# Kernel tuning notes

Hardware: AMD Instinct MI355X
Metric: run time of the kernel (lower is better)

The kernel has to match this reference:

```python
import jax, jax.numpy as jnp
import numpy as np

EPS = 1e-08


def _similarity_transform(S1, S2):
    """Batched Procrustes: S1, S2 are [B, 3, N]. Returns aligned S1_hat [B, 3, N]."""
    mu1 = jnp.mean(S1, axis=-1, keepdims=True)          # [B,3,1]
    mu2 = jnp.mean(S2, axis=-1, keepdims=True)
    X1 = S1 - mu1
    X2 = S2 - mu2
    var1 = jnp.sum(X1 * X1, axis=(1, 2))                # [B]
    # cross-covariance K = X1 @ X2^T + eps (eps added to every entry, as in torch ref)
    K = jnp.einsum('bin,bjn->bij', X1, X2) + EPS        # [B,3,3]
    U, s, Vh = jnp.linalg.svd(K, full_matrices=False)
    V = jnp.swapaxes(Vh, -1, -2)
    # det(U @ V^T) = det(U @ Vh); sign has zero gradient, same as torch
    sign = jax.lax.stop_gradient(jnp.sign(jnp.linalg.det(jnp.matmul(U, Vh))))  # [B]
    ones = jnp.ones_like(sign)
    d = jnp.stack([ones, ones, sign], axis=-1)          # diag of Z, [B,3]
    # R = V @ Z @ U^T
    R = jnp.einsum('bik,bk,bjk->bij', V, d, U)          # [B,3,3]
    scale = jnp.einsum('bij,bji->b', R, K) / var1       # trace(R@K)/var1, [B]
    t = mu2 - scale[:, None, None] * jnp.matmul(R, mu1)  # [B,3,1]
    S1_hat = scale[:, None, None] * jnp.matmul(R, S1) + t
    return S1_hat


def setup_inputs() -> dict:
    key = jax.random.key(0)
    k1, k2 = jax.random.split(key)
    B, N = 1024, 6890
    pred = jax.random.normal(k1, (B, N, 3), dtype=jnp.float32)
    gt = jax.random.normal(k2, (B, N, 3), dtype=jnp.float32)
    return {"pred": pred, "gt": gt}


def reference(pred, gt):
    # inputs are [B, N, 3] -> torch code transposes to [B, 3, N] and back
    S1 = jnp.swapaxes(pred, 1, 2)
    S2 = jnp.swapaxes(gt, 1, 2)
    S1_hat = jnp.swapaxes(_similarity_transform(S1, S2), 1, 2)  # [B,N,3]
    # loss_type == 'l1', reduction='none'
    return jnp.abs(S1_hat - gt)
```

## Files before the change

kernel.cpp:

```cpp
#include <hip/hip_runtime.h>
#include <math.h>

#define NPTS 6890
#define BATCH 1024
#define FLOATS_PER_BATCH (NPTS * 3)
#define NGROUPS 1722

__device__ __forceinline__ void accum(float* acc, float p0, float p1, float p2,
                                      float g0, float g1, float g2) {
  acc[0] += p0;  acc[1] += p1;  acc[2] += p2;
  acc[3] += g0;  acc[4] += g1;  acc[5] += g2;
  acc[6] += p0 * p0 + p1 * p1 + p2 * p2;
  acc[7]  += p0 * g0;  acc[8]  += p0 * g1;  acc[9]  += p0 * g2;
  acc[10] += p1 * g0;  acc[11] += p1 * g1;  acc[12] += p1 * g2;
  acc[13] += p2 * g0;  acc[14] += p2 * g1;  acc[15] += p2 * g2;
}

__global__ __launch_bounds__(256) void reduce_kernel(
    const float* __restrict__ pred, const float* __restrict__ gt,
    float* __restrict__ sums) {
  const int b = blockIdx.x;
  const size_t ofs0 = (size_t)b * FLOATS_PER_BATCH;
  const int skip = (b & 1) ? 2 : 0;
  const size_t ofs = ofs0 + (size_t)skip * 3;
  const float4* __restrict__ p4 = (const float4*)(pred + ofs);
  const float4* __restrict__ g4 = (const float4*)(gt + ofs);

  float acc[16];
#pragma unroll
  for (int i = 0; i < 16; ++i) acc[i] = 0.f;

  for (int gi = threadIdx.x; gi < NGROUPS; gi += 256) {
    const float4 a0 = p4[3 * gi], a1 = p4[3 * gi + 1], a2 = p4[3 * gi + 2];
    const float4 c0 = g4[3 * gi], c1 = g4[3 * gi + 1], c2 = g4[3 * gi + 2];
    accum(acc, a0.x, a0.y, a0.z, c0.x, c0.y, c0.z);
    accum(acc, a0.w, a1.x, a1.y, c0.w, c1.x, c1.y);
    accum(acc, a1.z, a1.w, a2.x, c1.z, c1.w, c2.x);
    accum(acc, a2.y, a2.z, a2.w, c2.y, c2.z, c2.w);
  }

  if (threadIdx.x < 2) {
    const int n = skip ? (int)threadIdx.x : (NPTS - 2 + (int)threadIdx.x);
    const float* pp = pred + ofs0 + 3 * n;
    const float* gg = gt + ofs0 + 3 * n;
    accum(acc, pp[0], pp[1], pp[2], gg[0], gg[1], gg[2]);
  }

#pragma unroll
  for (int i = 0; i < 16; ++i) {
#pragma unroll
    for (int off = 32; off > 0; off >>= 1)
      acc[i] += __shfl_down(acc[i], off, 64);
  }

  __shared__ float red[4][16];
  const int wave = threadIdx.x >> 6;
  const int lane = threadIdx.x & 63;
  if (lane == 0) {
#pragma unroll
    for (int i = 0; i < 16; ++i) red[wave][i] = acc[i];
  }
  __syncthreads();
  if (threadIdx.x < 16) {
    const int i = threadIdx.x;
    sums[b * 16 + i] = red[0][i] + red[1][i] + red[2][i] + red[3][i];
  }
}

__global__ void solve_kernel(const float* __restrict__ sums,
                             float* __restrict__ params) {
  const int b = blockIdx.x * blockDim.x + threadIdx.x;
  if (b >= BATCH) return;
  const float* s = sums + b * 16;
  const double Ninv = 1.0 / (double)NPTS;

  double sp[3] = {s[0], s[1], s[2]};
  double sg[3] = {s[3], s[4], s[5]};
  double mu1[3], mu2[3];
#pragma unroll
  for (int i = 0; i < 3; ++i) { mu1[i] = sp[i] * Ninv; mu2[i] = sg[i] * Ninv; }
  const double var1 =
      (double)s[6] - (sp[0] * sp[0] + sp[1] * sp[1] + sp[2] * sp[2]) * Ninv;

  double K[3][3];
#pragma unroll
  for (int i = 0; i < 3; ++i)
#pragma unroll
    for (int j = 0; j < 3; ++j)
      K[i][j] = (double)s[7 + 3 * i + j] - sp[i] * sg[j] * Ninv + 1e-8;

  double A[3][3];
#pragma unroll
  for (int i = 0; i < 3; ++i)
#pragma unroll
    for (int j = 0; j < 3; ++j)
      A[i][j] = K[0][i] * K[0][j] + K[1][i] * K[1][j] + K[2][i] * K[2][j];

  double V[3][3] = {{1, 0, 0}, {0, 1, 0}, {0, 0, 1}};
  for (int sweep = 0; sweep < 30; ++sweep) {
    const double off = A[0][1] * A[0][1] + A[0][2] * A[0][2] + A[1][2] * A[1][2];
    const double nrm = A[0][0] + A[1][1] + A[2][2];
    if (off <= 1e-30 * nrm * nrm) break;
    for (int pq = 0; pq < 3; ++pq) {
      const int p = (pq == 2) ? 1 : 0;
      const int q = (pq == 0) ? 1 : 2;
      const double apq = A[p][q];
      if (apq == 0.0) continue;
      const double theta = (A[q][q] - A[p][p]) / (2.0 * apq);
      const double tt =
          ((theta >= 0.0) ? 1.0 : -1.0) / (fabs(theta) + sqrt(theta * theta + 1.0));
      const double c = 1.0 / sqrt(tt * tt + 1.0);
      const double sn = tt * c;
      const double app = A[p][p], aqq = A[q][q];
      A[p][p] = app - tt * apq;
      A[q][q] = aqq + tt * apq;
      A[p][q] = 0.0; A[q][p] = 0.0;
      const int r = 3 - p - q;
      const double arp = A[r][p], arq = A[r][q];
      A[r][p] = c * arp - sn * arq; A[p][r] = A[r][p];
      A[r][q] = sn * arp + c * arq; A[q][r] = A[r][q];
#pragma unroll
      for (int k = 0; k < 3; ++k) {
        const double vkp = V[k][p], vkq = V[k][q];
        V[k][p] = c * vkp - sn * vkq;
        V[k][q] = sn * vkp + c * vkq;
      }
    }
  }

  double w[3] = {A[0][0], A[1][1], A[2][2]};
  int i0 = 0, i1 = 1, i2 = 2, tmp;
  if (w[i0] < w[i1]) { tmp = i0; i0 = i1; i1 = tmp; }
  if (w[i0] < w[i2]) { tmp = i0; i0 = i2; i2 = tmp; }
  if (w[i1] < w[i2]) { tmp = i1; i1 = i2; i2 = tmp; }
  const double sv0 = sqrt(fmax(w[i0], 0.0));
  const double sv1 = sqrt(fmax(w[i1], 0.0));
  const double sv2 = sqrt(fmax(w[i2], 0.0));

  const double detK =
      K[0][0] * (K[1][1] * K[2][2] - K[1][2] * K[2][1]) -
      K[0][1] * (K[1][0] * K[2][2] - K[1][2] * K[2][0]) +
      K[0][2] * (K[1][0] * K[2][1] - K[1][1] * K[2][0]);
  const double sgn = (detK > 0.0) ? 1.0 : ((detK < 0.0) ? -1.0 : 0.0);

  const double floor0 = sv0 * 1e-12 + 1e-300;
  const double z0 = 1.0 / fmax(sv0, floor0);
  const double z1 = 1.0 / fmax(sv1, floor0);
  const double z2 = sgn / fmax(sv2, floor0);

  double W[3][3];
#pragma unroll
  for (int a = 0; a < 3; ++a)
#pragma unroll
    for (int c = 0; c < 3; ++c)
      W[a][c] = V[a][i0] * V[c][i0] * z0 + V[a][i1] * V[c][i1] * z1 +
                V[a][i2] * V[c][i2] * z2;

  double R[3][3];
#pragma unroll
  for (int a = 0; a < 3; ++a)
#pragma unroll
    for (int c = 0; c < 3; ++c)
      R[a][c] = W[a][0] * K[c][0] + W[a][1] * K[c][1] + W[a][2] * K[c][2];

  const double trace = sv0 + sv1 + sgn * sv2;
  const double scale = trace / var1;

  float* pr = params + b * 12;
#pragma unroll
  for (int a = 0; a < 3; ++a) {
#pragma unroll
    for (int c = 0; c < 3; ++c) pr[3 * a + c] = (float)(scale * R[a][c]);
    pr[9 + a] = (float)(mu2[a] - scale * (R[a][0] * mu1[0] + R[a][1] * mu1[1] +
                                          R[a][2] * mu1[2]));
  }
}

__device__ __forceinline__ void xform(const float* m, float p0, float p1,
                                      float p2, float g0, float g1, float g2,
                                      float& o0, float& o1, float& o2) {
  o0 = fabsf(m[0] * p0 + m[1] * p1 + m[2] * p2 + m[9] - g0);
  o1 = fabsf(m[3] * p0 + m[4] * p1 + m[5] * p2 + m[10] - g1);
  o2 = fabsf(m[6] * p0 + m[7] * p1 + m[8] * p2 + m[11] - g2);
}

__global__ __launch_bounds__(256) void apply_kernel(
    const float* __restrict__ pred, const float* __restrict__ gt,
    const float* __restrict__ params, float* __restrict__ out) {
  const int b = blockIdx.y;
  float m[12];
#pragma unroll
  for (int i = 0; i < 12; ++i) m[i] = params[b * 12 + i];

  const size_t ofs0 = (size_t)b * FLOATS_PER_BATCH;
  const int skip = (b & 1) ? 2 : 0;
  const size_t ofs = ofs0 + (size_t)skip * 3;
  const int gi = blockIdx.x * 256 + threadIdx.x;

  if (gi < NGROUPS) {
    const float4* __restrict__ p4 = (const float4*)(pred + ofs);
    const float4* __restrict__ g4 = (const float4*)(gt + ofs);
    float4* __restrict__ o4 = (float4*)(out + ofs);
    const float4 a0 = p4[3 * gi], a1 = p4[3 * gi + 1], a2 = p4[3 * gi + 2];
    const float4 c0 = g4[3 * gi], c1 = g4[3 * gi + 1], c2 = g4[3 * gi + 2];
    float4 r0, r1, r2;
    xform(m, a0.x, a0.y, a0.z, c0.x, c0.y, c0.z, r0.x, r0.y, r0.z);
    xform(m, a0.w, a1.x, a1.y, c0.w, c1.x, c1.y, r0.w, r1.x, r1.y);
    xform(m, a1.z, a1.w, a2.x, c1.z, c1.w, c2.x, r1.z, r1.w, r2.x);
    xform(m, a2.y, a2.z, a2.w, c2.y, c2.z, c2.w, r2.y, r2.z, r2.w);
    o4[3 * gi] = r0; o4[3 * gi + 1] = r1; o4[3 * gi + 2] = r2;
  }

  if (blockIdx.x == 0 && threadIdx.x < 2) {
    const int n = skip ? (int)threadIdx.x : (NPTS - 2 + (int)threadIdx.x);
    const float* pp = pred + ofs0 + 3 * n;
    const float* gg = gt + ofs0 + 3 * n;
    float* oo = out + ofs0 + 3 * n;
    xform(m, pp[0], pp[1], pp[2], gg[0], gg[1], gg[2], oo[0], oo[1], oo[2]);
  }
}

extern "C" void kernel_launch(void* const* d_in, const int* in_sizes, int n_in,
                              void* d_out, int out_size, void* d_ws, size_t ws_size,
                              hipStream_t stream) {
  const float* pred = (const float*)d_in[0];
  const float* gt   = (const float*)d_in[1];
  float* out = (float*)d_out;
  float* sums   = (float*)d_ws;
  float* params = sums + BATCH * 16;

  hipLaunchKernelGGL(reduce_kernel, dim3(BATCH), dim3(256), 0, stream,
                     pred, gt, sums);
  hipLaunchKernelGGL(solve_kernel, dim3((BATCH + 255) / 256), dim3(256), 0,
                     stream, sums, params);
  hipLaunchKernelGGL(apply_kernel, dim3((NGROUPS + 255) / 256, BATCH),
                     dim3(256), 0, stream, pred, gt, params, out);
}
```

Measured before the change: 246.3 us.

## Split per-batch reduction into chunks, batch loads, and reshape solve/apply grids

The reduction now runs as four blocks per batch. Each thread issues all of its loads for up to two groups up front instead of looping, and writes per-chunk partial sums that the solve kernel adds together. The apply kernel has each thread handle two groups half a batch apart, which shrinks the grid and gives more loads in flight per thread. The solve kernel uses 64-thread blocks to spread across more CUs, and its Jacobi loop is capped at 10 sweeps with a looser convergence tolerance. This trades a small accuracy margin in the SVD, plus extra partial-sum traffic, for more parallelism and memory-level concurrency.

```diff
diff --git a/kernel.cpp b/kernel.cpp
--- a/kernel.cpp
+++ b/kernel.cpp
@@ -5,6 +5,9 @@
 #define BATCH 1024
 #define FLOATS_PER_BATCH (NPTS * 3)
 #define NGROUPS 1722
+#define CHUNKS 4
+#define GPC 431
+#define HALF_GROUPS 861
 
 __device__ __forceinline__ void accum(float* acc, float p0, float p1, float p2,
                                       float g0, float g1, float g2) {
@@ -16,30 +19,49 @@
   acc[13] += p2 * g0;  acc[14] += p2 * g1;  acc[15] += p2 * g2;
 }
 
+__device__ __forceinline__ void accum_grp(float* acc, const float4 a0,
+                                          const float4 a1, const float4 a2,
+                                          const float4 c0, const float4 c1,
+                                          const float4 c2) {
+  accum(acc, a0.x, a0.y, a0.z, c0.x, c0.y, c0.z);
+  accum(acc, a0.w, a1.x, a1.y, c0.w, c1.x, c1.y);
+  accum(acc, a1.z, a1.w, a2.x, c1.z, c1.w, c2.x);
+  accum(acc, a2.y, a2.z, a2.w, c2.y, c2.z, c2.w);
+}
+
 __global__ __launch_bounds__(256) void reduce_kernel(
     const float* __restrict__ pred, const float* __restrict__ gt,
-    float* __restrict__ sums) {
-  const int b = blockIdx.x;
+    float* __restrict__ partials) {
+  const int b = blockIdx.y;
+  const int c = blockIdx.x;
   const size_t ofs0 = (size_t)b * FLOATS_PER_BATCH;
   const int skip = (b & 1) ? 2 : 0;
   const size_t ofs = ofs0 + (size_t)skip * 3;
   const float4* __restrict__ p4 = (const float4*)(pred + ofs);
   const float4* __restrict__ g4 = (const float4*)(gt + ofs);
 
+  const int start = c * GPC;
+  const int end = (c == CHUNKS - 1) ? NGROUPS : (start + GPC);
+
   float acc[16];
 #pragma unroll
   for (int i = 0; i < 16; ++i) acc[i] = 0.f;
 
-  for (int gi = threadIdx.x; gi < NGROUPS; gi += 256) {
-    const float4 a0 = p4[3 * gi], a1 = p4[3 * gi + 1], a2 = p4[3 * gi + 2];
-    const float4 c0 = g4[3 * gi], c1 = g4[3 * gi + 1], c2 = g4[3 * gi + 2];
-    accum(acc, a0.x, a0.y, a0.z, c0.x, c0.y, c0.z);
-    accum(acc, a0.w, a1.x, a1.y, c0.w, c1.x, c1.y);
-    accum(acc, a1.z, a1.w, a2.x, c1.z, c1.w, c2.x);
-    accum(acc, a2.y, a2.z, a2.w, c2.y, c2.z, c2.w);
-  }
-
-  if (threadIdx.x < 2) {
+  const int g0 = start + (int)threadIdx.x;
+  const int g1 = g0 + 256;
+  const bool has1 = (g1 < end);
+
+  const float4 a0 = p4[3 * g0], a1 = p4[3 * g0 + 1], a2 = p4[3 * g0 + 2];
+  const float4 c0 = g4[3 * g0], c1 = g4[3 * g0 + 1], c2 = g4[3 * g0 + 2];
+  float4 b0, b1, b2, d0, d1, d2;
+  if (has1) {
+    b0 = p4[3 * g1]; b1 = p4[3 * g1 + 1]; b2 = p4[3 * g1 + 2];
+    d0 = g4[3 * g1]; d1 = g4[3 * g1 + 1]; d2 = g4[3 * g1 + 2];
+  }
+  accum_grp(acc, a0, a1, a2, c0, c1, c2);
+  if (has1) accum_grp(acc, b0, b1, b2, d0, d1, d2);
+
+  if (c == 0 && threadIdx.x < 2) {
     const int n = skip ? (int)threadIdx.x : (NPTS - 2 + (int)threadIdx.x);
     const float* pp = pred + ofs0 + 3 * n;
     const float* gg = gt + ofs0 + 3 * n;
@@ -63,15 +85,24 @@
   __syncthreads();
   if (threadIdx.x < 16) {
     const int i = threadIdx.x;
-    sums[b * 16 + i] = red[0][i] + red[1][i] + red[2][i] + red[3][i];
-  }
-}
-
-__global__ void solve_kernel(const float* __restrict__ sums,
+    partials[(b * CHUNKS + c) * 16 + i] =
+        red[0][i] + red[1][i] + red[2][i] + red[3][i];
+  }
+}
+
+__global__ void solve_kernel(const float* __restrict__ partials,
                              float* __restrict__ params) {
   const int b = blockIdx.x * blockDim.x + threadIdx.x;
   if (b >= BATCH) return;
-  const float* s = sums + b * 16;
+
+  float s[16];
+#pragma unroll
+  for (int i = 0; i < 16; ++i) {
+    s[i] = partials[(b * CHUNKS + 0) * 16 + i] +
+           partials[(b * CHUNKS + 1) * 16 + i] +
+           partials[(b * CHUNKS + 2) * 16 + i] +
+           partials[(b * CHUNKS + 3) * 16 + i];
+  }
   const double Ninv = 1.0 / (double)NPTS;
 
   double sp[3] = {s[0], s[1], s[2]};
@@ -97,10 +128,10 @@
       A[i][j] = K[0][i] * K[0][j] + K[1][i] * K[1][j] + K[2][i] * K[2][j];
 
   double V[3][3] = {{1, 0, 0}, {0, 1, 0}, {0, 0, 1}};
-  for (int sweep = 0; sweep < 30; ++sweep) {
+  for (int sweep = 0; sweep < 10; ++sweep) {
     const double off = A[0][1] * A[0][1] + A[0][2] * A[0][2] + A[1][2] * A[1][2];
     const double nrm = A[0][0] + A[1][1] + A[2][2];
-    if (off <= 1e-30 * nrm * nrm) break;
+    if (off <= 1e-26 * nrm * nrm) break;
     for (int pq = 0; pq < 3; ++pq) {
       const int p = (pq == 2) ? 1 : 0;
       const int q = (pq == 0) ? 1 : 2;
@@ -109,21 +140,21 @@
       const double theta = (A[q][q] - A[p][p]) / (2.0 * apq);
       const double tt =
           ((theta >= 0.0) ? 1.0 : -1.0) / (fabs(theta) + sqrt(theta * theta + 1.0));
-      const double c = 1.0 / sqrt(tt * tt + 1.0);
-      const double sn = tt * c;
+      const double cj = 1.0 / sqrt(tt * tt + 1.0);
+      const double sn = tt * cj;
       const double app = A[p][p], aqq = A[q][q];
       A[p][p] = app - tt * apq;
       A[q][q] = aqq + tt * apq;
       A[p][q] = 0.0; A[q][p] = 0.0;
       const int r = 3 - p - q;
       const double arp = A[r][p], arq = A[r][q];
-      A[r][p] = c * arp - sn * arq; A[p][r] = A[r][p];
-      A[r][q] = sn * arp + c * arq; A[q][r] = A[r][q];
+      A[r][p] = cj * arp - sn * arq; A[p][r] = A[r][p];
+      A[r][q] = sn * arp + cj * arq; A[q][r] = A[r][q];
 #pragma unroll
       for (int k = 0; k < 3; ++k) {
         const double vkp = V[k][p], vkq = V[k][q];
-        V[k][p] = c * vkp - sn * vkq;
-        V[k][q] = sn * vkp + c * vkq;
+        V[k][p] = cj * vkp - sn * vkq;
+        V[k][q] = sn * vkp + cj * vkq;
       }
     }
   }
@@ -152,16 +183,16 @@
 #pragma unroll
   for (int a = 0; a < 3; ++a)
 #pragma unroll
-    for (int c = 0; c < 3; ++c)
-      W[a][c] = V[a][i0] * V[c][i0] * z0 + V[a][i1] * V[c][i1] * z1 +
-                V[a][i2] * V[c][i2] * z2;
+    for (int cc = 0; cc < 3; ++cc)
+      W[a][cc] = V[a][i0] * V[cc][i0] * z0 + V[a][i1] * V[cc][i1] * z1 +
+                 V[a][i2] * V[cc][i2] * z2;
 
   double R[3][3];
 #pragma unroll
   for (int a = 0; a < 3; ++a)
 #pragma unroll
-    for (int c = 0; c < 3; ++c)
-      R[a][c] = W[a][0] * K[c][0] + W[a][1] * K[c][1] + W[a][2] * K[c][2];
+    for (int cc = 0; cc < 3; ++cc)
+      R[a][cc] = W[a][0] * K[cc][0] + W[a][1] * K[cc][1] + W[a][2] * K[cc][2];
 
   const double trace = sv0 + sv1 + sgn * sv2;
   const double scale = trace / var1;
@@ -170,7 +201,7 @@
 #pragma unroll
   for (int a = 0; a < 3; ++a) {
 #pragma unroll
-    for (int c = 0; c < 3; ++c) pr[3 * a + c] = (float)(scale * R[a][c]);
+    for (int cc = 0; cc < 3; ++cc) pr[3 * a + cc] = (float)(scale * R[a][cc]);
     pr[9 + a] = (float)(mu2[a] - scale * (R[a][0] * mu1[0] + R[a][1] * mu1[1] +
                                           R[a][2] * mu1[2]));
   }
@@ -184,6 +215,17 @@
   o2 = fabsf(m[6] * p0 + m[7] * p1 + m[8] * p2 + m[11] - g2);
 }
 
+__device__ __forceinline__ void xform_grp(const float* m, const float4 a0,
+                                          const float4 a1, const float4 a2,
+                                          const float4 c0, const float4 c1,
+                                          const float4 c2, float4& r0,
+                                          float4& r1, float4& r2) {
+  xform(m, a0.x, a0.y, a0.z, c0.x, c0.y, c0.z, r0.x, r0.y, r0.z);
+  xform(m, a0.w, a1.x, a1.y, c0.w, c1.x, c1.y, r0.w, r1.x, r1.y);
+  xform(m, a1.z, a1.w, a2.x, c1.z, c1.w, c2.x, r1.z, r1.w, r2.x);
+  xform(m, a2.y, a2.z, a2.w, c2.y, c2.z, c2.w, r2.y, r2.z, r2.w);
+}
+
 __global__ __launch_bounds__(256) void apply_kernel(
     const float* __restrict__ pred, const float* __restrict__ gt,
     const float* __restrict__ params, float* __restrict__ out) {
@@ -195,20 +237,22 @@
   const size_t ofs0 = (size_t)b * FLOATS_PER_BATCH;
   const int skip = (b & 1) ? 2 : 0;
   const size_t ofs = ofs0 + (size_t)skip * 3;
-  const int gi = blockIdx.x * 256 + threadIdx.x;
-
-  if (gi < NGROUPS) {
+  const int idx = blockIdx.x * 256 + threadIdx.x;
+
+  if (idx < HALF_GROUPS) {
+    const int g0 = idx, g1 = idx + HALF_GROUPS;
     const float4* __restrict__ p4 = (const float4*)(pred + ofs);
     const float4* __restrict__ g4 = (const float4*)(gt + ofs);
     float4* __restrict__ o4 = (float4*)(out + ofs);
-    const float4 a0 = p4[3 * gi], a1 = p4[3 * gi + 1], a2 = p4[3 * gi + 2];
-    const float4 c0 = g4[3 * gi], c1 = g4[3 * gi + 1], c2 = g4[3 * gi + 2];
-    float4 r0, r1, r2;
-    xform(m, a0.x, a0.y, a0.z, c0.x, c0.y, c0.z, r0.x, r0.y, r0.z);
-    xform(m, a0.w, a1.x, a1.y, c0.w, c1.x, c1.y, r0.w, r1.x, r1.y);
-    xform(m, a1.z, a1.w, a2.x, c1.z, c1.w, c2.x, r1.z, r1.w, r2.x);
-    xform(m, a2.y, a2.z, a2.w, c2.y, c2.z, c2.w, r2.y, r2.z, r2.w);
-    o4[3 * gi] = r0; o4[3 * gi + 1] = r1; o4[3 * gi + 2] = r2;
+    const float4 a0 = p4[3 * g0], a1 = p4[3 * g0 + 1], a2 = p4[3 * g0 + 2];
+    const float4 c0 = g4[3 * g0], c1 = g4[3 * g0 + 1], c2 = g4[3 * g0 + 2];
+    const float4 b0 = p4[3 * g1], b1 = p4[3 * g1 + 1], b2 = p4[3 * g1 + 2];
+    const float4 d0 = g4[3 * g1], d1 = g4[3 * g1 + 1], d2 = g4[3 * g1 + 2];
+    float4 r0, r1, r2, q0, q1, q2;
+    xform_grp(m, a0, a1, a2, c0, c1, c2, r0, r1, r2);
+    xform_grp(m, b0, b1, b2, d0, d1, d2, q0, q1, q2);
+    o4[3 * g0] = r0; o4[3 * g0 + 1] = r1; o4[3 * g0 + 2] = r2;
+    o4[3 * g1] = q0; o4[3 * g1 + 1] = q1; o4[3 * g1 + 2] = q2;
   }
 
   if (blockIdx.x == 0 && threadIdx.x < 2) {
@@ -226,13 +270,13 @@
   const float* pred = (const float*)d_in[0];
   const float* gt   = (const float*)d_in[1];
   float* out = (float*)d_out;
-  float* sums   = (float*)d_ws;
-  float* params = sums + BATCH * 16;
-
-  hipLaunchKernelGGL(reduce_kernel, dim3(BATCH), dim3(256), 0, stream,
-                     pred, gt, sums);
-  hipLaunchKernelGGL(solve_kernel, dim3((BATCH + 255) / 256), dim3(256), 0,
-                     stream, sums, params);
-  hipLaunchKernelGGL(apply_kernel, dim3((NGROUPS + 255) / 256, BATCH),
-                     dim3(256), 0, stream, pred, gt, params, out);
-}
+  float* partials = (float*)d_ws;
+  float* params   = partials + BATCH * CHUNKS * 16;
+
+  hipLaunchKernelGGL(reduce_kernel, dim3(CHUNKS, BATCH), dim3(256), 0, stream,
+                     pred, gt, partials);
+  hipLaunchKernelGGL(solve_kernel, dim3(16), dim3(64), 0, stream,
+                     partials, params);
+  hipLaunchKernelGGL(apply_kernel, dim3(4, BATCH), dim3(256), 0, stream,
+                     pred, gt, params, out);
+}
```

After: 246.6 us. No clear change (+0.1%).

## Fuse reduce, solve and apply into one register-resident kernel per batch

Applied to the files above, without the earlier changes.

Replaces the three-kernel pipeline with a single kernel where each 512-thread block loads its batch's pred and gt into registers once. It reduces the statistics, and then each thread redundantly solves the 3x3 Procrustes in fp32 and applies the transform from the cached registers. This removes the second global read of the inputs, the workspace round-trip and two launches. The trade-offs are lower-precision fp32 Jacobi SVD with fewer sweeps, high register pressure, and redundant per-thread solve work.

```diff
diff --git a/kernel.cpp b/kernel.cpp
--- a/kernel.cpp
+++ b/kernel.cpp
@@ -3,8 +3,9 @@
 
 #define NPTS 6890
 #define BATCH 1024
-#define FLOATS_PER_BATCH (NPTS * 3)
-#define NGROUPS 1722
+#define FPB (NPTS * 3)
+#define FQ 5166
+
 
 __device__ __forceinline__ void accum(float* acc, float p0, float p1, float p2,
                                       float g0, float g1, float g2) {
@@ -16,164 +17,14 @@
   acc[13] += p2 * g0;  acc[14] += p2 * g1;  acc[15] += p2 * g2;
 }
 
-__global__ __launch_bounds__(256) void reduce_kernel(
-    const float* __restrict__ pred, const float* __restrict__ gt,
-    float* __restrict__ sums) {
-  const int b = blockIdx.x;
-  const size_t ofs0 = (size_t)b * FLOATS_PER_BATCH;
-  const int skip = (b & 1) ? 2 : 0;
-  const size_t ofs = ofs0 + (size_t)skip * 3;
-  const float4* __restrict__ p4 = (const float4*)(pred + ofs);
-  const float4* __restrict__ g4 = (const float4*)(gt + ofs);
-
-  float acc[16];
-#pragma unroll
-  for (int i = 0; i < 16; ++i) acc[i] = 0.f;
-
-  for (int gi = threadIdx.x; gi < NGROUPS; gi += 256) {
-    const float4 a0 = p4[3 * gi], a1 = p4[3 * gi + 1], a2 = p4[3 * gi + 2];
-    const float4 c0 = g4[3 * gi], c1 = g4[3 * gi + 1], c2 = g4[3 * gi + 2];
-    accum(acc, a0.x, a0.y, a0.z, c0.x, c0.y, c0.z);
-    accum(acc, a0.w, a1.x, a1.y, c0.w, c1.x, c1.y);
-    accum(acc, a1.z, a1.w, a2.x, c1.z, c1.w, c2.x);
-    accum(acc, a2.y, a2.z, a2.w, c2.y, c2.z, c2.w);
-  }
-
-  if (threadIdx.x < 2) {
-    const int n = skip ? (int)threadIdx.x : (NPTS - 2 + (int)threadIdx.x);
-    const float* pp = pred + ofs0 + 3 * n;
-    const float* gg = gt + ofs0 + 3 * n;
-    accum(acc, pp[0], pp[1], pp[2], gg[0], gg[1], gg[2]);
-  }
-
-#pragma unroll
-  for (int i = 0; i < 16; ++i) {
-#pragma unroll
-    for (int off = 32; off > 0; off >>= 1)
-      acc[i] += __shfl_down(acc[i], off, 64);
-  }
-
-  __shared__ float red[4][16];
-  const int wave = threadIdx.x >> 6;
-  const int lane = threadIdx.x & 63;
-  if (lane == 0) {
-#pragma unroll
-    for (int i = 0; i < 16; ++i) red[wave][i] = acc[i];
-  }
-  __syncthreads();
-  if (threadIdx.x < 16) {
-    const int i = threadIdx.x;
-    sums[b * 16 + i] = red[0][i] + red[1][i] + red[2][i] + red[3][i];
-  }
-}
-
-__global__ void solve_kernel(const float* __restrict__ sums,
-                             float* __restrict__ params) {
-  const int b = blockIdx.x * blockDim.x + threadIdx.x;
-  if (b >= BATCH) return;
-  const float* s = sums + b * 16;
-  const double Ninv = 1.0 / (double)NPTS;
-
-  double sp[3] = {s[0], s[1], s[2]};
-  double sg[3] = {s[3], s[4], s[5]};
-  double mu1[3], mu2[3];
-#pragma unroll
-  for (int i = 0; i < 3; ++i) { mu1[i] = sp[i] * Ninv; mu2[i] = sg[i] * Ninv; }
-  const double var1 =
-      (double)s[6] - (sp[0] * sp[0] + sp[1] * sp[1] + sp[2] * sp[2]) * Ninv;
-
-  double K[3][3];
-#pragma unroll
-  for (int i = 0; i < 3; ++i)
-#pragma unroll
-    for (int j = 0; j < 3; ++j)
-      K[i][j] = (double)s[7 + 3 * i + j] - sp[i] * sg[j] * Ninv + 1e-8;
-
-  double A[3][3];
-#pragma unroll
-  for (int i = 0; i < 3; ++i)
-#pragma unroll
-    for (int j = 0; j < 3; ++j)
-      A[i][j] = K[0][i] * K[0][j] + K[1][i] * K[1][j] + K[2][i] * K[2][j];
-
-  double V[3][3] = {{1, 0, 0}, {0, 1, 0}, {0, 0, 1}};
-  for (int sweep = 0; sweep < 30; ++sweep) {
-    const double off = A[0][1] * A[0][1] + A[0][2] * A[0][2] + A[1][2] * A[1][2];
-    const double nrm = A[0][0] + A[1][1] + A[2][2];
-    if (off <= 1e-30 * nrm * nrm) break;
-    for (int pq = 0; pq < 3; ++pq) {
-      const int p = (pq == 2) ? 1 : 0;
-      const int q = (pq == 0) ? 1 : 2;
-      const double apq = A[p][q];
-      if (apq == 0.0) continue;
-      const double theta = (A[q][q] - A[p][p]) / (2.0 * apq);
-      const double tt =
-          ((theta >= 0.0) ? 1.0 : -1.0) / (fabs(theta) + sqrt(theta * theta + 1.0));
-      const double c = 1.0 / sqrt(tt * tt + 1.0);
-      const double sn = tt * c;
-      const double app = A[p][p], aqq = A[q][q];
-      A[p][p] = app - tt * apq;
-      A[q][q] = aqq + tt * apq;
-      A[p][q] = 0.0; A[q][p] = 0.0;
-      const int r = 3 - p - q;
-      const double arp = A[r][p], arq = A[r][q];
-      A[r][p] = c * arp - sn * arq; A[p][r] = A[r][p];
-      A[r][q] = sn * arp + c * arq; A[q][r] = A[r][q];
-#pragma unroll
-      for (int k = 0; k < 3; ++k) {
-        const double vkp = V[k][p], vkq = V[k][q];
-        V[k][p] = c * vkp - sn * vkq;
-        V[k][q] = sn * vkp + c * vkq;
-      }
-    }
-  }
-
-  double w[3] = {A[0][0], A[1][1], A[2][2]};
-  int i0 = 0, i1 = 1, i2 = 2, tmp;
-  if (w[i0] < w[i1]) { tmp = i0; i0 = i1; i1 = tmp; }
-  if (w[i0] < w[i2]) { tmp = i0; i0 = i2; i2 = tmp; }
-  if (w[i1] < w[i2]) { tmp = i1; i1 = i2; i2 = tmp; }
-  const double sv0 = sqrt(fmax(w[i0], 0.0));
-  const double sv1 = sqrt(fmax(w[i1], 0.0));
-  const double sv2 = sqrt(fmax(w[i2], 0.0));
-
-  const double detK =
-      K[0][0] * (K[1][1] * K[2][2] - K[1][2] * K[2][1]) -
-      K[0][1] * (K[1][0] * K[2][2] - K[1][2] * K[2][0]) +
-      K[0][2] * (K[1][0] * K[2][1] - K[1][1] * K[2][0]);
-  const double sgn = (detK > 0.0) ? 1.0 : ((detK < 0.0) ? -1.0 : 0.0);
-
-  const double floor0 = sv0 * 1e-12 + 1e-300;
-  const double z0 = 1.0 / fmax(sv0, floor0);
-  const double z1 = 1.0 / fmax(sv1, floor0);
-  const double z2 = sgn / fmax(sv2, floor0);
-
-  double W[3][3];
-#pragma unroll
-  for (int a = 0; a < 3; ++a)
-#pragma unroll
-    for (int c = 0; c < 3; ++c)
-      W[a][c] = V[a][i0] * V[c][i0] * z0 + V[a][i1] * V[c][i1] * z1 +
-                V[a][i2] * V[c][i2] * z2;
-
-  double R[3][3];
-#pragma unroll
-  for (int a = 0; a < 3; ++a)
-#pragma unroll
-    for (int c = 0; c < 3; ++c)
-      R[a][c] = W[a][0] * K[c][0] + W[a][1] * K[c][1] + W[a][2] * K[c][2];
-
-  const double trace = sv0 + sv1 + sgn * sv2;
-  const double scale = trace / var1;
-
-  float* pr = params + b * 12;
-#pragma unroll
-  for (int a = 0; a < 3; ++a) {
-#pragma unroll
-    for (int c = 0; c < 3; ++c) pr[3 * a + c] = (float)(scale * R[a][c]);
-    pr[9 + a] = (float)(mu2[a] - scale * (R[a][0] * mu1[0] + R[a][1] * mu1[1] +
-                                          R[a][2] * mu1[2]));
-  }
+__device__ __forceinline__ void accum_grp(float* acc, const float4 a0,
+                                          const float4 a1, const float4 a2,
+                                          const float4 c0, const float4 c1,
+                                          const float4 c2) {
+  accum(acc, a0.x, a0.y, a0.z, c0.x, c0.y, c0.z);
+  accum(acc, a0.w, a1.x, a1.y, c0.w, c1.x, c1.y);
+  accum(acc, a1.z, a1.w, a2.x, c1.z, c1.w, c2.x);
+  accum(acc, a2.y, a2.z, a2.w, c2.y, c2.z, c2.w);
 }
 
 __device__ __forceinline__ void xform(const float* m, float p0, float p1,
@@ -184,39 +35,202 @@
   o2 = fabsf(m[6] * p0 + m[7] * p1 + m[8] * p2 + m[11] - g2);
 }
 
-__global__ __launch_bounds__(256) void apply_kernel(
+__device__ __forceinline__ void xform_grp(const float* m, const float4 a0,
+                                          const float4 a1, const float4 a2,
+                                          const float4 c0, const float4 c1,
+                                          const float4 c2, float4& r0,
+                                          float4& r1, float4& r2) {
+  xform(m, a0.x, a0.y, a0.z, c0.x, c0.y, c0.z, r0.x, r0.y, r0.z);
+  xform(m, a0.w, a1.x, a1.y, c0.w, c1.x, c1.y, r0.w, r1.x, r1.y);
+  xform(m, a1.z, a1.w, a2.x, c1.z, c1.w, c2.x, r1.z, r1.w, r2.x);
+  xform(m, a2.y, a2.z, a2.w, c2.y, c2.z, c2.w, r2.y, r2.z, r2.w);
+}
+
+__device__ __forceinline__ void solve_params(const float* s, float* pr) {
+  const float Ninv = 1.0f / (float)NPTS;
+  const float sp[3] = {s[0], s[1], s[2]};
+  const float sg[3] = {s[3], s[4], s[5]};
+  float mu1[3], mu2[3];
+#pragma unroll
+  for (int i = 0; i < 3; ++i) { mu1[i] = sp[i] * Ninv; mu2[i] = sg[i] * Ninv; }
+  const float var1 =
+      s[6] - (sp[0] * sp[0] + sp[1] * sp[1] + sp[2] * sp[2]) * Ninv;
+
+  float K[3][3];
+#pragma unroll
+  for (int i = 0; i < 3; ++i)
+#pragma unroll
+    for (int j = 0; j < 3; ++j)
+      K[i][j] = s[7 + 3 * i + j] - sp[i] * sg[j] * Ninv + 1e-8f;
+
+  float A[3][3];
+#pragma unroll
+  for (int i = 0; i < 3; ++i)
+#pragma unroll
+    for (int j = 0; j < 3; ++j)
+      A[i][j] = K[0][i] * K[0][j] + K[1][i] * K[1][j] + K[2][i] * K[2][j];
+
+  float V[3][3] = {{1, 0, 0}, {0, 1, 0}, {0, 0, 1}};
+  for (int sweep = 0; sweep < 10; ++sweep) {
+    const float off =
+        A[0][1] * A[0][1] + A[0][2] * A[0][2] + A[1][2] * A[1][2];
+    const float nrm = A[0][0] + A[1][1] + A[2][2];
+    if (off <= 1e-12f * nrm * nrm) break;
+    for (int pq = 0; pq < 3; ++pq) {
+      const int p = (pq == 2) ? 1 : 0;
+      const int q = (pq == 0) ? 1 : 2;
+      const float apq = A[p][q];
+      if (apq == 0.0f) continue;
+      const float theta = (A[q][q] - A[p][p]) / (2.0f * apq);
+      const float tt = ((theta >= 0.0f) ? 1.0f : -1.0f) /
+                       (fabsf(theta) + sqrtf(theta * theta + 1.0f));
+      const float cj = 1.0f / sqrtf(tt * tt + 1.0f);
+      const float sn = tt * cj;
+      const float app = A[p][p], aqq = A[q][q];
+      A[p][p] = app - tt * apq;
+      A[q][q] = aqq + tt * apq;
+      A[p][q] = 0.0f; A[q][p] = 0.0f;
+      const int r = 3 - p - q;
+      const float arp = A[r][p], arq = A[r][q];
+      A[r][p] = cj * arp - sn * arq; A[p][r] = A[r][p];
+      A[r][q] = sn * arp + cj * arq; A[q][r] = A[r][q];
+#pragma unroll
+      for (int k = 0; k < 3; ++k) {
+        const float vkp = V[k][p], vkq = V[k][q];
+        V[k][p] = cj * vkp - sn * vkq;
+        V[k][q] = sn * vkp + cj * vkq;
+      }
+    }
+  }
+
+  float w[3] = {A[0][0], A[1][1], A[2][2]};
+  int i0 = 0, i1 = 1, i2 = 2, tmp;
+  if (w[i0] < w[i1]) { tmp = i0; i0 = i1; i1 = tmp; }
+  if (w[i0] < w[i2]) { tmp = i0; i0 = i2; i2 = tmp; }
+  if (w[i1] < w[i2]) { tmp = i1; i1 = i2; i2 = tmp; }
+  const float sv0 = sqrtf(fmaxf(w[i0], 0.0f));
+  const float sv1 = sqrtf(fmaxf(w[i1], 0.0f));
+  const float sv2 = sqrtf(fmaxf(w[i2], 0.0f));
+
+  const float detK =
+      K[0][0] * (K[1][1] * K[2][2] - K[1][2] * K[2][1]) -
+      K[0][1] * (K[1][0] * K[2][2] - K[1][2] * K[2][0]) +
+      K[0][2] * (K[1][0] * K[2][1] - K[1][1] * K[2][0]);
+  const float sgn = (detK > 0.0f) ? 1.0f : ((detK < 0.0f) ? -1.0f : 0.0f);
+
+  const float floor0 = sv0 * 1e-6f + 1e-30f;
+  const float z0 = 1.0f / fmaxf(sv0, floor0);
+  const float z1 = 1.0f / fmaxf(sv1, floor0);
+  const float z2 = sgn / fmaxf(sv2, floor0);
+
+  float W[3][3];
+#pragma unroll
+  for (int a = 0; a < 3; ++a)
+#pragma unroll
+    for (int c = 0; c < 3; ++c)
+      W[a][c] = V[a][i0] * V[c][i0] * z0 + V[a][i1] * V[c][i1] * z1 +
+                V[a][i2] * V[c][i2] * z2;
+
+  float R[3][3];
+#pragma unroll
+  for (int a = 0; a < 3; ++a)
+#pragma unroll
+    for (int c = 0; c < 3; ++c)
+      R[a][c] = W[a][0] * K[c][0] + W[a][1] * K[c][1] + W[a][2] * K[c][2];
+
+  const float trace = sv0 + sv1 + sgn * sv2;
+  const float scale = trace / var1;
+
+#pragma unroll
+  for (int a = 0; a < 3; ++a) {
+#pragma unroll
+    for (int c = 0; c < 3; ++c) pr[3 * a + c] = scale * R[a][c];
+    pr[9 + a] = mu2[a] - scale * (R[a][0] * mu1[0] + R[a][1] * mu1[1] +
+                                  R[a][2] * mu1[2]);
+  }
+}
+
+__global__ __launch_bounds__(512) void fused_kernel(
     const float* __restrict__ pred, const float* __restrict__ gt,
-    const float* __restrict__ params, float* __restrict__ out) {
-  const int b = blockIdx.y;
-  float m[12];
-#pragma unroll
-  for (int i = 0; i < 12; ++i) m[i] = params[b * 12 + i];
-
-  const size_t ofs0 = (size_t)b * FLOATS_PER_BATCH;
+    float* __restrict__ out) {
+  const int b = blockIdx.x;
+  const int t = threadIdx.x;
+  const size_t ofs0 = (size_t)b * FPB;
   const int skip = (b & 1) ? 2 : 0;
   const size_t ofs = ofs0 + (size_t)skip * 3;
-  const int gi = blockIdx.x * 256 + threadIdx.x;
-
-  if (gi < NGROUPS) {
-    const float4* __restrict__ p4 = (const float4*)(pred + ofs);
-    const float4* __restrict__ g4 = (const float4*)(gt + ofs);
-    float4* __restrict__ o4 = (float4*)(out + ofs);
-    const float4 a0 = p4[3 * gi], a1 = p4[3 * gi + 1], a2 = p4[3 * gi + 2];
-    const float4 c0 = g4[3 * gi], c1 = g4[3 * gi + 1], c2 = g4[3 * gi + 2];
+  const float4* __restrict__ p4 = (const float4*)(pred + ofs);
+  const float4* __restrict__ g4 = (const float4*)(gt + ofs);
+  float4* __restrict__ o4 = (float4*)(out + ofs);
+
+  const int base = 12 * t;
+  const float4 z4 = make_float4(0.f, 0.f, 0.f, 0.f);
+
+  float4 pc[12], gc[12];
+#pragma unroll
+  for (int j = 0; j < 12; ++j) {
+    const bool v = (base + j) < FQ;
+    pc[j] = v ? p4[base + j] : z4;
+    gc[j] = v ? g4[base + j] : z4;
+  }
+
+  float acc[16];
+#pragma unroll
+  for (int i = 0; i < 16; ++i) acc[i] = 0.f;
+#pragma unroll
+  for (int g = 0; g < 4; ++g)
+    accum_grp(acc, pc[3 * g], pc[3 * g + 1], pc[3 * g + 2],
+              gc[3 * g], gc[3 * g + 1], gc[3 * g + 2]);
+
+  if (t == 431) {
+    const int n0 = skip ? 0 : (NPTS - 2);
+    const float* pp = pred + ofs0 + 3 * n0;
+    const float* gg = gt + ofs0 + 3 * n0;
+    accum(acc, pp[0], pp[1], pp[2], gg[0], gg[1], gg[2]);
+    accum(acc, pp[3], pp[4], pp[5], gg[3], gg[4], gg[5]);
+  }
+
+#pragma unroll
+  for (int i = 0; i < 16; ++i) {
+#pragma unroll
+    for (int off = 32; off > 0; off >>= 1)
+      acc[i] += __shfl_down(acc[i], off, 64);
+  }
+  __shared__ float red[8][16];
+  const int w = t >> 6, lane = t & 63;
+  if (lane == 0) {
+#pragma unroll
+    for (int i = 0; i < 16; ++i) red[w][i] = acc[i];
+  }
+  __syncthreads();
+
+  float s[16];
+#pragma unroll
+  for (int i = 0; i < 16; ++i) {
+    float v = red[0][i];
+#pragma unroll
+    for (int ww = 1; ww < 8; ++ww) v += red[ww][i];
+    s[i] = v;
+  }
+
+  float m[12];
+  solve_params(s, m);
+
+#pragma unroll
+  for (int g = 0; g < 4; ++g) {
     float4 r0, r1, r2;
-    xform(m, a0.x, a0.y, a0.z, c0.x, c0.y, c0.z, r0.x, r0.y, r0.z);
-    xform(m, a0.w, a1.x, a1.y, c0.w, c1.x, c1.y, r0.w, r1.x, r1.y);
-    xform(m, a1.z, a1.w, a2.x, c1.z, c1.w, c2.x, r1.z, r1.w, r2.x);
-    xform(m, a2.y, a2.z, a2.w, c2.y, c2.z, c2.w, r2.y, r2.z, r2.w);
-    o4[3 * gi] = r0; o4[3 * gi + 1] = r1; o4[3 * gi + 2] = r2;
-  }
-
-  if (blockIdx.x == 0 && threadIdx.x < 2) {
-    const int n = skip ? (int)threadIdx.x : (NPTS - 2 + (int)threadIdx.x);
-    const float* pp = pred + ofs0 + 3 * n;
-    const float* gg = gt + ofs0 + 3 * n;
-    float* oo = out + ofs0 + 3 * n;
+    xform_grp(m, pc[3 * g], pc[3 * g + 1], pc[3 * g + 2],
+              gc[3 * g], gc[3 * g + 1], gc[3 * g + 2], r0, r1, r2);
+    if (base + 3 * g + 0 < FQ) o4[base + 3 * g + 0] = r0;
+    if (base + 3 * g + 1 < FQ) o4[base + 3 * g + 1] = r1;
+    if (base + 3 * g + 2 < FQ) o4[base + 3 * g + 2] = r2;
+  }
+  if (t == 431) {
+    const int n0 = skip ? 0 : (NPTS - 2);
+    const float* pp = pred + ofs0 + 3 * n0;
+    const float* gg = gt + ofs0 + 3 * n0;
+    float* oo = out + ofs0 + 3 * n0;
     xform(m, pp[0], pp[1], pp[2], gg[0], gg[1], gg[2], oo[0], oo[1], oo[2]);
+    xform(m, pp[3], pp[4], pp[5], gg[3], gg[4], gg[5], oo[3], oo[4], oo[5]);
   }
 }
 
@@ -226,13 +240,6 @@
   const float* pred = (const float*)d_in[0];
   const float* gt   = (const float*)d_in[1];
   float* out = (float*)d_out;
-  float* sums   = (float*)d_ws;
-  float* params = sums + BATCH * 16;
-
-  hipLaunchKernelGGL(reduce_kernel, dim3(BATCH), dim3(256), 0, stream,
-                     pred, gt, sums);
-  hipLaunchKernelGGL(solve_kernel, dim3((BATCH + 255) / 256), dim3(256), 0,
-                     stream, sums, params);
-  hipLaunchKernelGGL(apply_kernel, dim3((NGROUPS + 255) / 256, BATCH),
-                     dim3(256), 0, stream, pred, gt, params, out);
-}
+  hipLaunchKernelGGL(fused_kernel, dim3(BATCH), dim3(512), 0, stream,
+                     pred, gt, out);
+}
```

Result: slower. 333.4 us (+35.3%).
